# Kernel optimization log

Measured on AMD Instinct MI355X. Metric: run time of the kernel, lower is better.

Reference implementation:

```python
import jax, jax.numpy as jnp
import numpy as np

WH, WW = 7, 7
NUM_HEADS = 12


def _relative_position_index(wh, ww):
    coords = np.stack(np.meshgrid(np.arange(wh), np.arange(ww), indexing='ij'))  # (2,wh,ww)
    flat = coords.reshape(2, -1)                       # (2, N)
    rel = flat[:, :, None] - flat[:, None, :]          # (2, N, N)
    rel = rel.transpose(1, 2, 0).astype(np.int64)      # (N, N, 2)
    rel[..., 0] += wh - 1
    rel[..., 1] += ww - 1
    rel[..., 0] *= 2 * ww - 1
    return rel.sum(-1)                                 # (N, N)


REL_IDX = _relative_position_index(WH, WW)


def setup_inputs() -> dict:
    key = jax.random.key(0)
    ks = jax.random.split(key, 5)
    B_, N, C = 2048, WH * WW, 384
    nW = 256
    return {
        'x': jax.random.normal(ks[0], (B_, N, C), jnp.float32),
        'input_shape': 8,  # (B,H,W,C) placeholder; only used by the conv proj path
        'mask': jax.random.normal(ks[1], (nW, N, N), jnp.float32),
        'Wqkv': jax.random.normal(ks[2], (C, 3 * C), jnp.float32) * 0.02,
        'bqkv': jnp.zeros((3 * C,), jnp.float32),
        'bias_table': jax.random.normal(ks[3], ((2 * WH - 1) * (2 * WW - 1), NUM_HEADS), jnp.float32) * 0.02,
        'Wproj': jax.random.normal(ks[4], (C, C), jnp.float32) * 0.02,
        'bproj': jnp.zeros((C,), jnp.float32),
    }


def reference(x, input_shape, mask, Wqkv, bqkv, bias_table, Wproj, bproj):
    B_, N, C = x.shape
    H = NUM_HEADS
    hd = C // H
    scale = hd ** (-0.5)
    # linear qkv projection
    qkv = x @ Wqkv + bqkv                                  # (B_, N, 3C)
    qkv = qkv.reshape(B_, N, 3, H, hd).transpose(2, 0, 3, 1, 4)
    q, k, v = qkv[0] * scale, qkv[1], qkv[2]               # (B_, H, N, hd)
    attn = jnp.einsum('bhnd,bhmd->bhnm', q, k)             # (B_, H, N, N)
    # relative position bias gather
    bias = bias_table[REL_IDX.reshape(-1)].reshape(N, N, H).transpose(2, 0, 1)
    attn = attn + bias[None]
    # additive window mask
    nW = mask.shape[0]
    attn = attn.reshape(B_ // nW, nW, H, N, N) + mask[None, :, None]
    attn = jax.nn.softmax(attn.reshape(B_, H, N, N), axis=-1)
    out = jnp.einsum('bhnm,bhmd->bhnd', attn, v)           # (B_, H, N, hd)
    out = out.transpose(0, 2, 1, 3).reshape(B_, N, C)
    out = out @ Wproj + bproj
    return out, attn
```

## Files before the change

kernel.cpp:

```cpp
#include <hip/hip_runtime.h>
#include <math.h>

#define WH 7
#define WW 7
#define NN 49
#define HEADS 12
#define HD 32
#define CC 384
#define NW 256

typedef short s16x8 __attribute__((ext_vector_type(8)));
typedef unsigned short u16x8 __attribute__((ext_vector_type(8)));
typedef float f32x4 __attribute__((ext_vector_type(4)));

__device__ __forceinline__ unsigned short f2bf(float x) {
  unsigned u = __builtin_bit_cast(unsigned, x);
  u += 0x7fffu + ((u >> 16) & 1u);
  return (unsigned short)(u >> 16);
}
__device__ __forceinline__ float bf2f(unsigned short b) {
  unsigned u = ((unsigned)b) << 16;
  return __builtin_bit_cast(float, u);
}

__global__ void split_wt_kernel(const float* __restrict__ W,
                                unsigned short* __restrict__ Th,
                                unsigned short* __restrict__ Tl,
                                int K, int N) {
  const int idx = blockIdx.x * 256 + threadIdx.x;
  if (idx >= K * N) return;
  const int k = idx / N, n = idx % N;
  const float v = W[idx];
  const unsigned short h = f2bf(v);
  const size_t t = (size_t)n * K + k;
  Th[t] = h;
  Tl[t] = f2bf(v - bf2f(h));
}

template <bool NT>
__global__ __launch_bounds__(256) void gemm_bf16x3_kernel(
    const float* __restrict__ A, const unsigned short* __restrict__ Bth,
    const unsigned short* __restrict__ Btl, const float* __restrict__ bias,
    float* __restrict__ C, int M, int N, int K, int tilesN, int chunk) {
  __shared__ unsigned short Ash[128][40];
  __shared__ unsigned short Asl[128][40];
  __shared__ unsigned short Bsh[128][40];
  __shared__ unsigned short Bsl[128][40];

  const int lin = blockIdx.x;
  const int logical = (lin & 7) * chunk + (lin >> 3);
  const int bm = (logical / tilesN) * 128;
  const int bn = (logical % tilesN) * 128;

  const int tid = threadIdx.x;
  const int lane = tid & 63;
  const int wv = tid >> 6;
  const int wm = (wv >> 1) * 64;
  const int wn = (wv & 1) * 64;
  const int fr = lane & 15;
  const int g8 = (lane >> 4) * 8;

  const int srow = tid >> 1;
  const int sc16 = (tid & 1) * 16;

  f32x4 acc[4][4] = {};

  for (int k0 = 0; k0 < K; k0 += 32) {
    {
      const float* src = &A[(size_t)(bm + srow) * K + k0 + sc16];
      float v[16];
      *(f32x4*)&v[0] = *(const f32x4*)&src[0];
      *(f32x4*)&v[4] = *(const f32x4*)&src[4];
      *(f32x4*)&v[8] = *(const f32x4*)&src[8];
      *(f32x4*)&v[12] = *(const f32x4*)&src[12];
      unsigned short h[16], l[16];
#pragma unroll
      for (int i = 0; i < 16; ++i) {
        h[i] = f2bf(v[i]);
        l[i] = f2bf(v[i] - bf2f(h[i]));
      }
      *(u16x8*)&Ash[srow][sc16] = *(u16x8*)&h[0];
      *(u16x8*)&Ash[srow][sc16 + 8] = *(u16x8*)&h[8];
      *(u16x8*)&Asl[srow][sc16] = *(u16x8*)&l[0];
      *(u16x8*)&Asl[srow][sc16 + 8] = *(u16x8*)&l[8];
    }
    {
      const size_t off = (size_t)(bn + srow) * K + k0 + sc16;
      const unsigned short* sh = &Bth[off];
      const unsigned short* sl = &Btl[off];
      *(u16x8*)&Bsh[srow][sc16] = *(const u16x8*)&sh[0];
      *(u16x8*)&Bsh[srow][sc16 + 8] = *(const u16x8*)&sh[8];
      *(u16x8*)&Bsl[srow][sc16] = *(const u16x8*)&sl[0];
      *(u16x8*)&Bsl[srow][sc16 + 8] = *(const u16x8*)&sl[8];
    }
    __syncthreads();

    s16x8 ah[4], al[4];
#pragma unroll
    for (int m = 0; m < 4; ++m) {
      ah[m] = *(const s16x8*)&Ash[wm + m * 16 + fr][g8];
      al[m] = *(const s16x8*)&Asl[wm + m * 16 + fr][g8];
    }
#pragma unroll
    for (int n = 0; n < 4; ++n) {
      const s16x8 bh = *(const s16x8*)&Bsh[wn + n * 16 + fr][g8];
      const s16x8 bl = *(const s16x8*)&Bsl[wn + n * 16 + fr][g8];
#pragma unroll
      for (int m = 0; m < 4; ++m) {
        acc[m][n] = __builtin_amdgcn_mfma_f32_16x16x32_bf16(ah[m], bh,
                                                            acc[m][n], 0, 0, 0);
        acc[m][n] = __builtin_amdgcn_mfma_f32_16x16x32_bf16(ah[m], bl,
                                                            acc[m][n], 0, 0, 0);
        acc[m][n] = __builtin_amdgcn_mfma_f32_16x16x32_bf16(al[m], bh,
                                                            acc[m][n], 0, 0, 0);
      }
    }
    __syncthreads();
  }

  const int r0 = (lane >> 4) * 4;
#pragma unroll
  for (int m = 0; m < 4; ++m) {
#pragma unroll
    for (int r = 0; r < 4; ++r) {
      const int row = bm + wm + m * 16 + r0 + r;
      float* dst = &C[(size_t)row * N + bn + wn];
#pragma unroll
      for (int n = 0; n < 4; ++n) {
        const float val = acc[m][n][r] + bias[bn + wn + n * 16 + fr];
        if (NT)
          __builtin_nontemporal_store(val, &dst[n * 16 + fr]);
        else
          dst[n * 16 + fr] = val;
      }
    }
  }
}

__global__ __launch_bounds__(256) void attn_fused_kernel(
    const float* __restrict__ qkv, const float* __restrict__ mask,
    const float* __restrict__ bias_table, float* __restrict__ attn_out,
    float* __restrict__ o_buf) {
  const int b = blockIdx.x / HEADS;
  const int h = blockIdx.x % HEADS;
  const int tid = threadIdx.x;

  __shared__ float qs[NN][HD + 1];
  __shared__ float ks[NN][HD + 1];
  __shared__ float vs[NN][HD + 1];
  __shared__ float S[NN][NN + 4];
  __shared__ float rinv[NN];

  const float scale = 0.17677669529663687f;

  for (int idx = tid; idx < NN * (HD / 4); idx += 256) {
    const int n = idx / (HD / 4);
    const int d4 = (idx % (HD / 4)) * 4;
    const size_t base = ((size_t)(b * NN + n) * 3) * CC + h * HD + d4;
    const float4 qv = *reinterpret_cast<const float4*>(&qkv[base]);
    const float4 kv = *reinterpret_cast<const float4*>(&qkv[base + CC]);
    const float4 vv = *reinterpret_cast<const float4*>(&qkv[base + 2 * CC]);
    qs[n][d4 + 0] = qv.x * scale; qs[n][d4 + 1] = qv.y * scale;
    qs[n][d4 + 2] = qv.z * scale; qs[n][d4 + 3] = qv.w * scale;
    ks[n][d4 + 0] = kv.x; ks[n][d4 + 1] = kv.y;
    ks[n][d4 + 2] = kv.z; ks[n][d4 + 3] = kv.w;
    vs[n][d4 + 0] = vv.x; vs[n][d4 + 1] = vv.y;
    vs[n][d4 + 2] = vv.z; vs[n][d4 + 3] = vv.w;
  }
  __syncthreads();

  const float* mrow = &mask[(size_t)(b % NW) * NN * NN];
  for (int idx = tid; idx < NN * NN; idx += 256) {
    const int i = idx / NN, j = idx % NN;
    float s = 0.f;
#pragma unroll
    for (int d = 0; d < HD; ++d) s = fmaf(qs[i][d], ks[j][d], s);
    const int ih = i / WW, iw = i % WW, jh = j / WW, jw = j % WW;
    const int rel = (ih - jh + WH - 1) * (2 * WW - 1) + (iw - jw + WW - 1);
    s += bias_table[rel * HEADS + h] + mrow[idx];
    S[i][j] = s;
  }
  __syncthreads();

  if (tid < 4 * NN) {
    const int i = tid >> 2, t = tid & 3;
    float m = -1e30f;
    for (int j = t; j < NN; j += 4) m = fmaxf(m, S[i][j]);
    m = fmaxf(m, __shfl_xor(m, 1));
    m = fmaxf(m, __shfl_xor(m, 2));
    float sum = 0.f;
    for (int j = t; j < NN; j += 4) {
      const float e = __expf(S[i][j] - m);
      S[i][j] = e;
      sum += e;
    }
    sum += __shfl_xor(sum, 1);
    sum += __shfl_xor(sum, 2);
    if (t == 0) rinv[i] = 1.0f / sum;
  }
  __syncthreads();

  float* aout = &attn_out[(size_t)blockIdx.x * NN * NN];
  for (int idx = tid; idx < NN * NN; idx += 256) {
    const int i = idx / NN, j = idx % NN;
    const float p = S[i][j] * rinv[i];
    S[i][j] = p;
    __builtin_nontemporal_store(p, &aout[idx]);
  }
  __syncthreads();

  for (int idx = tid; idx < NN * HD; idx += 256) {
    const int i = idx / HD, d = idx % HD;
    float acc = 0.f;
    for (int j = 0; j < NN; ++j) acc = fmaf(S[i][j], vs[j][d], acc);
    o_buf[((size_t)(b * NN) + i) * CC + h * HD + d] = acc;
  }
}

extern "C" void kernel_launch(void* const* d_in, const int* in_sizes, int n_in,
                              void* d_out, int out_size, void* d_ws,
                              size_t ws_size, hipStream_t stream) {
  const float* x = (const float*)d_in[0];
  const float* mask = (const float*)d_in[2];
  const float* Wqkv = (const float*)d_in[3];
  const float* bqkv = (const float*)d_in[4];
  const float* bias_table = (const float*)d_in[5];
  const float* Wproj = (const float*)d_in[6];
  const float* bproj = (const float*)d_in[7];

  const int B_ = in_sizes[0] / (NN * CC);
  const int M = B_ * NN;

  float* out = (float*)d_out;
  float* attn = out + (size_t)M * CC;

  float* qkv_buf = (float*)d_ws;
  float* o_buf = qkv_buf + (size_t)M * 3 * CC;
  unsigned short* wqkvt_h = (unsigned short*)(o_buf + (size_t)M * CC);
  unsigned short* wqkvt_l = wqkvt_h + (size_t)3 * CC * CC;
  unsigned short* wprojt_h = wqkvt_l + (size_t)3 * CC * CC;
  unsigned short* wprojt_l = wprojt_h + (size_t)CC * CC;

  split_wt_kernel<<<(3 * CC * CC + 255) / 256, 256, 0, stream>>>(
      Wqkv, wqkvt_h, wqkvt_l, CC, 3 * CC);
  split_wt_kernel<<<(CC * CC + 255) / 256, 256, 0, stream>>>(
      Wproj, wprojt_h, wprojt_l, CC, CC);

  {
    const int tilesM = M / 128, tilesN = (3 * CC) / 128;
    const int nwg = tilesM * tilesN;
    gemm_bf16x3_kernel<false><<<nwg, 256, 0, stream>>>(
        x, wqkvt_h, wqkvt_l, bqkv, qkv_buf, M, 3 * CC, CC, tilesN, nwg / 8);
  }
  {
    dim3 grid(B_ * HEADS);
    attn_fused_kernel<<<grid, 256, 0, stream>>>(qkv_buf, mask, bias_table,
                                                attn, o_buf);
  }
  {
    const int tilesM = M / 128, tilesN = CC / 128;
    const int nwg = tilesM * tilesN;
    gemm_bf16x3_kernel<true><<<nwg, 256, 0, stream>>>(
        o_buf, wprojt_h, wprojt_l, bproj, out, M, CC, CC, tilesN, nwg / 8);
  }
}
```

Measured before the change: 1.360 ms.

## Move window attention matmuls to MFMA bf16x3 and prefetch GEMM tiles into registers

The scalar attention kernel is replaced by an MFMA version. Q, K and V are split into bf16 hi/lo pairs in LDS and QK^T and PV are computed with three-term bf16 MFMAs, padded from 49 to 64. Softmax now runs in registers with cross-lane shuffles, which removes the fp32 score staging and several barriers. The GEMM kernel also loads the next K-slice of A and B into registers while the current one is being multiplied, to hide global load latency. The trade-offs are some wasted work on the padding, more register pressure, and bf16x3 accuracy in attention instead of fp32.

```diff
diff --git a/kernel.cpp b/kernel.cpp
--- a/kernel.cpp
+++ b/kernel.cpp
@@ -63,37 +63,58 @@
   const int srow = tid >> 1;
   const int sc16 = (tid & 1) * 16;
 
+  const float* aptr = &A[(size_t)(bm + srow) * K + sc16];
+  const unsigned short* bhp = &Bth[(size_t)(bn + srow) * K + sc16];
+  const unsigned short* blp = &Btl[(size_t)(bn + srow) * K + sc16];
+
+  f32x4 ar[4];
+  u16x8 brh[2], brl[2];
+  ar[0] = *(const f32x4*)&aptr[0];
+  ar[1] = *(const f32x4*)&aptr[4];
+  ar[2] = *(const f32x4*)&aptr[8];
+  ar[3] = *(const f32x4*)&aptr[12];
+  brh[0] = *(const u16x8*)&bhp[0];
+  brh[1] = *(const u16x8*)&bhp[8];
+  brl[0] = *(const u16x8*)&blp[0];
+  brl[1] = *(const u16x8*)&blp[8];
+
   f32x4 acc[4][4] = {};
 
   for (int k0 = 0; k0 < K; k0 += 32) {
     {
-      const float* src = &A[(size_t)(bm + srow) * K + k0 + sc16];
       float v[16];
-      *(f32x4*)&v[0] = *(const f32x4*)&src[0];
-      *(f32x4*)&v[4] = *(const f32x4*)&src[4];
-      *(f32x4*)&v[8] = *(const f32x4*)&src[8];
-      *(f32x4*)&v[12] = *(const f32x4*)&src[12];
-      unsigned short h[16], l[16];
+      *(f32x4*)&v[0] = ar[0];
+      *(f32x4*)&v[4] = ar[1];
+      *(f32x4*)&v[8] = ar[2];
+      *(f32x4*)&v[12] = ar[3];
+      unsigned short hh[16], ll[16];
 #pragma unroll
       for (int i = 0; i < 16; ++i) {
-        h[i] = f2bf(v[i]);
-        l[i] = f2bf(v[i] - bf2f(h[i]));
-      }
-      *(u16x8*)&Ash[srow][sc16] = *(u16x8*)&h[0];
-      *(u16x8*)&Ash[srow][sc16 + 8] = *(u16x8*)&h[8];
-      *(u16x8*)&Asl[srow][sc16] = *(u16x8*)&l[0];
-      *(u16x8*)&Asl[srow][sc16 + 8] = *(u16x8*)&l[8];
-    }
-    {
-      const size_t off = (size_t)(bn + srow) * K + k0 + sc16;
-      const unsigned short* sh = &Bth[off];
-      const unsigned short* sl = &Btl[off];
-      *(u16x8*)&Bsh[srow][sc16] = *(const u16x8*)&sh[0];
-      *(u16x8*)&Bsh[srow][sc16 + 8] = *(const u16x8*)&sh[8];
-      *(u16x8*)&Bsl[srow][sc16] = *(const u16x8*)&sl[0];
-      *(u16x8*)&Bsl[srow][sc16 + 8] = *(const u16x8*)&sl[8];
+        hh[i] = f2bf(v[i]);
+        ll[i] = f2bf(v[i] - bf2f(hh[i]));
+      }
+      *(u16x8*)&Ash[srow][sc16] = *(u16x8*)&hh[0];
+      *(u16x8*)&Ash[srow][sc16 + 8] = *(u16x8*)&hh[8];
+      *(u16x8*)&Asl[srow][sc16] = *(u16x8*)&ll[0];
+      *(u16x8*)&Asl[srow][sc16 + 8] = *(u16x8*)&ll[8];
+      *(u16x8*)&Bsh[srow][sc16] = brh[0];
+      *(u16x8*)&Bsh[srow][sc16 + 8] = brh[1];
+      *(u16x8*)&Bsl[srow][sc16] = brl[0];
+      *(u16x8*)&Bsl[srow][sc16 + 8] = brl[1];
     }
     __syncthreads();
+
+    if (k0 + 32 < K) {
+      const int kn = k0 + 32;
+      ar[0] = *(const f32x4*)&aptr[kn];
+      ar[1] = *(const f32x4*)&aptr[kn + 4];
+      ar[2] = *(const f32x4*)&aptr[kn + 8];
+      ar[3] = *(const f32x4*)&aptr[kn + 12];
+      brh[0] = *(const u16x8*)&bhp[kn];
+      brh[1] = *(const u16x8*)&bhp[kn + 8];
+      brl[0] = *(const u16x8*)&blp[kn];
+      brl[1] = *(const u16x8*)&blp[kn + 8];
+    }
 
     s16x8 ah[4], al[4];
 #pragma unroll
@@ -137,83 +158,141 @@
   }
 }
 
-__global__ __launch_bounds__(256) void attn_fused_kernel(
+__global__ __launch_bounds__(256) void attn_mfma_kernel(
     const float* __restrict__ qkv, const float* __restrict__ mask,
     const float* __restrict__ bias_table, float* __restrict__ attn_out,
     float* __restrict__ o_buf) {
   const int b = blockIdx.x / HEADS;
   const int h = blockIdx.x % HEADS;
   const int tid = threadIdx.x;
-
-  __shared__ float qs[NN][HD + 1];
-  __shared__ float ks[NN][HD + 1];
-  __shared__ float vs[NN][HD + 1];
-  __shared__ float S[NN][NN + 4];
-  __shared__ float rinv[NN];
+  const int lane = tid & 63;
+  const int wv = tid >> 6;
+  const int fr = lane & 15;
+  const int grp = lane >> 4;
+
+  __shared__ unsigned short qh[64][40], ql[64][40];
+  __shared__ unsigned short kh[64][40], kl[64][40];
+  __shared__ unsigned short vh[32][72], vl[32][72];
+  __shared__ unsigned short Ph[64][72], Pl[64][72];
 
   const float scale = 0.17677669529663687f;
 
   for (int idx = tid; idx < NN * (HD / 4); idx += 256) {
-    const int n = idx / (HD / 4);
-    const int d4 = (idx % (HD / 4)) * 4;
+    const int n = idx >> 3, d4 = (idx & 7) * 4;
     const size_t base = ((size_t)(b * NN + n) * 3) * CC + h * HD + d4;
     const float4 qv = *reinterpret_cast<const float4*>(&qkv[base]);
     const float4 kv = *reinterpret_cast<const float4*>(&qkv[base + CC]);
     const float4 vv = *reinterpret_cast<const float4*>(&qkv[base + 2 * CC]);
-    qs[n][d4 + 0] = qv.x * scale; qs[n][d4 + 1] = qv.y * scale;
-    qs[n][d4 + 2] = qv.z * scale; qs[n][d4 + 3] = qv.w * scale;
-    ks[n][d4 + 0] = kv.x; ks[n][d4 + 1] = kv.y;
-    ks[n][d4 + 2] = kv.z; ks[n][d4 + 3] = kv.w;
-    vs[n][d4 + 0] = vv.x; vs[n][d4 + 1] = vv.y;
-    vs[n][d4 + 2] = vv.z; vs[n][d4 + 3] = vv.w;
+    const float qa[4] = {qv.x * scale, qv.y * scale, qv.z * scale,
+                         qv.w * scale};
+    const float ka[4] = {kv.x, kv.y, kv.z, kv.w};
+    const float va[4] = {vv.x, vv.y, vv.z, vv.w};
+#pragma unroll
+    for (int c = 0; c < 4; ++c) {
+      unsigned short t;
+      t = f2bf(qa[c]); qh[n][d4 + c] = t; ql[n][d4 + c] = f2bf(qa[c] - bf2f(t));
+      t = f2bf(ka[c]); kh[n][d4 + c] = t; kl[n][d4 + c] = f2bf(ka[c] - bf2f(t));
+      t = f2bf(va[c]); vh[d4 + c][n] = t; vl[d4 + c][n] = f2bf(va[c] - bf2f(t));
+    }
+  }
+  for (int idx = tid; idx < 32 * 15; idx += 256) {
+    const int d = idx / 15, kk = NN + idx % 15;
+    vh[d][kk] = 0;
+    vl[d][kk] = 0;
   }
   __syncthreads();
 
+  f32x4 sacc[4] = {};
+  {
+    const s16x8 aqh = *(const s16x8*)&qh[wv * 16 + fr][grp * 8];
+    const s16x8 aql = *(const s16x8*)&ql[wv * 16 + fr][grp * 8];
+#pragma unroll
+    for (int n = 0; n < 4; ++n) {
+      const s16x8 bh = *(const s16x8*)&kh[n * 16 + fr][grp * 8];
+      const s16x8 bl = *(const s16x8*)&kl[n * 16 + fr][grp * 8];
+      sacc[n] = __builtin_amdgcn_mfma_f32_16x16x32_bf16(aqh, bh, sacc[n], 0, 0, 0);
+      sacc[n] = __builtin_amdgcn_mfma_f32_16x16x32_bf16(aqh, bl, sacc[n], 0, 0, 0);
+      sacc[n] = __builtin_amdgcn_mfma_f32_16x16x32_bf16(aql, bh, sacc[n], 0, 0, 0);
+    }
+  }
+
   const float* mrow = &mask[(size_t)(b % NW) * NN * NN];
-  for (int idx = tid; idx < NN * NN; idx += 256) {
-    const int i = idx / NN, j = idx % NN;
-    float s = 0.f;
-#pragma unroll
-    for (int d = 0; d < HD; ++d) s = fmaf(qs[i][d], ks[j][d], s);
-    const int ih = i / WW, iw = i % WW, jh = j / WW, jw = j % WW;
-    const int rel = (ih - jh + WH - 1) * (2 * WW - 1) + (iw - jw + WW - 1);
-    s += bias_table[rel * HEADS + h] + mrow[idx];
-    S[i][j] = s;
-  }
-  __syncthreads();
-
-  if (tid < 4 * NN) {
-    const int i = tid >> 2, t = tid & 3;
-    float m = -1e30f;
-    for (int j = t; j < NN; j += 4) m = fmaxf(m, S[i][j]);
+  const int rowbase = wv * 16 + grp * 4;
+  float sv[4][4];
+#pragma unroll
+  for (int n = 0; n < 4; ++n) {
+    const int col = n * 16 + fr;
+#pragma unroll
+    for (int r = 0; r < 4; ++r) {
+      const int row = rowbase + r;
+      float s = -1e30f;
+      if (row < NN && col < NN) {
+        const int rel = (row / WW - col / WW + WH - 1) * (2 * WW - 1) +
+                        (row % WW - col % WW + WW - 1);
+        s = sacc[n][r] + bias_table[rel * HEADS + h] + mrow[row * NN + col];
+      }
+      sv[n][r] = s;
+    }
+  }
+
+  float* aout = &attn_out[(size_t)blockIdx.x * NN * NN];
+#pragma unroll
+  for (int r = 0; r < 4; ++r) {
+    float m = fmaxf(fmaxf(sv[0][r], sv[1][r]), fmaxf(sv[2][r], sv[3][r]));
     m = fmaxf(m, __shfl_xor(m, 1));
     m = fmaxf(m, __shfl_xor(m, 2));
-    float sum = 0.f;
-    for (int j = t; j < NN; j += 4) {
-      const float e = __expf(S[i][j] - m);
-      S[i][j] = e;
-      sum += e;
+    m = fmaxf(m, __shfl_xor(m, 4));
+    m = fmaxf(m, __shfl_xor(m, 8));
+    float p[4], sum = 0.f;
+#pragma unroll
+    for (int n = 0; n < 4; ++n) {
+      p[n] = __expf(sv[n][r] - m);
+      sum += p[n];
     }
     sum += __shfl_xor(sum, 1);
     sum += __shfl_xor(sum, 2);
-    if (t == 0) rinv[i] = 1.0f / sum;
+    sum += __shfl_xor(sum, 4);
+    sum += __shfl_xor(sum, 8);
+    const float rinv = 1.0f / sum;
+    const int row = rowbase + r;
+#pragma unroll
+    for (int n = 0; n < 4; ++n) {
+      const float pv = p[n] * rinv;
+      const int col = n * 16 + fr;
+      if (row < NN && col < NN)
+        __builtin_nontemporal_store(pv, &aout[row * NN + col]);
+      const unsigned short t = f2bf(pv);
+      Ph[row][col] = t;
+      Pl[row][col] = f2bf(pv - bf2f(t));
+    }
   }
   __syncthreads();
 
-  float* aout = &attn_out[(size_t)blockIdx.x * NN * NN];
-  for (int idx = tid; idx < NN * NN; idx += 256) {
-    const int i = idx / NN, j = idx % NN;
-    const float p = S[i][j] * rinv[i];
-    S[i][j] = p;
-    __builtin_nontemporal_store(p, &aout[idx]);
-  }
-  __syncthreads();
-
-  for (int idx = tid; idx < NN * HD; idx += 256) {
-    const int i = idx / HD, d = idx % HD;
-    float acc = 0.f;
-    for (int j = 0; j < NN; ++j) acc = fmaf(S[i][j], vs[j][d], acc);
-    o_buf[((size_t)(b * NN) + i) * CC + h * HD + d] = acc;
+  f32x4 oacc[2] = {};
+#pragma unroll
+  for (int kk = 0; kk < 2; ++kk) {
+    const s16x8 pah = *(const s16x8*)&Ph[wv * 16 + fr][kk * 32 + grp * 8];
+    const s16x8 pal = *(const s16x8*)&Pl[wv * 16 + fr][kk * 32 + grp * 8];
+#pragma unroll
+    for (int n = 0; n < 2; ++n) {
+      const s16x8 vbh = *(const s16x8*)&vh[n * 16 + fr][kk * 32 + grp * 8];
+      const s16x8 vbl = *(const s16x8*)&vl[n * 16 + fr][kk * 32 + grp * 8];
+      oacc[n] = __builtin_amdgcn_mfma_f32_16x16x32_bf16(pah, vbh, oacc[n], 0, 0, 0);
+      oacc[n] = __builtin_amdgcn_mfma_f32_16x16x32_bf16(pah, vbl, oacc[n], 0, 0, 0);
+      oacc[n] = __builtin_amdgcn_mfma_f32_16x16x32_bf16(pal, vbh, oacc[n], 0, 0, 0);
+    }
+  }
+
+#pragma unroll
+  for (int n = 0; n < 2; ++n) {
+#pragma unroll
+    for (int r = 0; r < 4; ++r) {
+      const int row = rowbase + r;
+      if (row < NN) {
+        o_buf[((size_t)(b * NN) + row) * CC + h * HD + n * 16 + fr] =
+            oacc[n][r];
+      }
+    }
   }
 }
 
@@ -254,8 +333,8 @@
   }
   {
     dim3 grid(B_ * HEADS);
-    attn_fused_kernel<<<grid, 256, 0, stream>>>(qkv_buf, mask, bias_table,
-                                                attn, o_buf);
+    attn_mfma_kernel<<<grid, 256, 0, stream>>>(qkv_buf, mask, bias_table, attn,
+                                               o_buf);
   }
   {
     const int tilesM = M / 128, tilesN = CC / 128;
```

After: 1.181 ms. -13.2%, faster.
